# Optimization experiments

Measured on AMD Instinct MI355X. Metric: run time of the kernel, lower is better.

## Reference

```python
import jax, jax.numpy as jnp
import numpy as np

NUM_FREQS = 10
Z_SIZE = 256
HIDDEN = 256
N_LAYERS = 8
N_POLY = 100000
PE_DIM = 2 * NUM_FREQS + 2 * NUM_FREQS * 2 + 4  # 64
IN1 = PE_DIM + Z_SIZE        # 320
IN_MID = HIDDEN + IN1        # 576
SLOPE = 0.01


def setup_inputs() -> dict:
    key = jax.random.key(0)
    ks = jax.random.split(key, 12)
    B = 131072
    xy = jax.random.normal(ks[0], (B, 2), dtype=jnp.float32)
    idx = jax.random.randint(ks[1], (B,), 0, N_POLY, dtype=jnp.int64 if jax.config.jax_enable_x64 else jnp.int32)
    emb = jax.random.normal(ks[2], (N_POLY, Z_SIZE), dtype=jnp.float32) * 0.01
    s = 0.02
    W1a = jax.random.normal(ks[3], (IN1, HIDDEN), dtype=jnp.float32) * s
    b1a = jnp.zeros((HIDDEN,), jnp.float32)
    W1b = jax.random.normal(ks[4], (HIDDEN, HIDDEN), dtype=jnp.float32) * s
    b1b = jnp.zeros((HIDDEN,), jnp.float32)
    Wa = jax.random.normal(ks[5], (N_LAYERS, IN_MID, HIDDEN), dtype=jnp.float32) * s
    ba = jnp.zeros((N_LAYERS, HIDDEN), jnp.float32)
    Wb = jax.random.normal(ks[6], (N_LAYERS, HIDDEN, HIDDEN), dtype=jnp.float32) * s
    bb = jnp.zeros((N_LAYERS, HIDDEN), jnp.float32)
    W2 = jax.random.normal(ks[7], (HIDDEN, 1), dtype=jnp.float32) * s
    b2 = jnp.zeros((1,), jnp.float32)
    return {"xy": xy, "idx": idx, "emb": emb, "W1a": W1a, "b1a": b1a,
            "W1b": W1b, "b1b": b1b, "Wa": Wa, "ba": ba, "Wb": Wb, "bb": bb,
            "W2": W2, "b2": b2}


def _pos_encode(xy):
    # linspace freq bands (log_sampling=False default)
    freq = jnp.linspace(1.0, 6.0, NUM_FREQS).astype(xy.dtype)  # (F,)
    xf = xy[:, None, :] * freq[:, None]                         # (B,F,2)
    # cat([x_input, sin, cos], dim=1) then reshape -> (B, (1+2F)*2)
    out = jnp.concatenate([xy[:, None, :], jnp.sin(xf), jnp.cos(xf)], axis=1)
    out = out.reshape(xy.shape[0], -1)                          # (B,42)
    # polar fourier encoding
    r = jnp.sqrt(xy[:, 0] ** 2 + xy[:, 1] ** 2)                 # (B,)
    rf = r[:, None] * freq                                      # (B,F)
    pe = jnp.concatenate([xy, jnp.sin(rf), jnp.cos(rf)], axis=-1)  # (B,22)
    return jnp.concatenate([out, pe], axis=-1)                  # (B,64)


def reference(xy, idx, emb, W1a, b1a, W1b, b1b, Wa, ba, Wb, bb, W2, b2):
    feat = _pos_encode(xy)                       # (B,64)
    z = emb[idx]                                 # (B,256)
    xy_z = jnp.concatenate([feat, z], axis=1)    # (B,320)
    x = jax.nn.leaky_relu(xy_z @ W1a + b1a, SLOPE) @ W1b + b1b  # (B,256)
    for i in range(N_LAYERS):
        h = jnp.concatenate([xy_z, x], axis=1)   # (B,576)
        x = jax.nn.leaky_relu(h @ Wa[i] + ba[i], SLOPE) @ Wb[i] + bb[i]
    return x @ W2 + b2                           # (B,1)
```

## Files before the change

### kernel.cpp

```cpp
#include <hip/hip_runtime.h>
#include <hip/hip_bf16.h>


typedef __attribute__((ext_vector_type(8))) __bf16 bfv8;
typedef __attribute__((ext_vector_type(8))) short s16x8;
typedef __attribute__((ext_vector_type(4))) float f32x4;
typedef __attribute__((ext_vector_type(4))) int i32x4;

__device__ __forceinline__ short f2bf(float f) {
  unsigned u = __builtin_bit_cast(unsigned, f);
  u = (u + 0x7fffu + ((u >> 16) & 1u)) >> 16;
  return (short)u;
}
__device__ __forceinline__ float bf2f(short s) {
  unsigned u = ((unsigned)(unsigned short)s) << 16;
  return __builtin_bit_cast(float, u);
}
__device__ __forceinline__ int swzaddr(int base, int stride, int row, int colbyte) {
  return base + row * stride + (colbyte ^ (((row & 7) << 4) ^ ((row & 8) << 2)));
}
__device__ __forceinline__ void ldsbar() {
  __builtin_amdgcn_sched_barrier(0);
  asm volatile("s_waitcnt lgkmcnt(0)");
  __builtin_amdgcn_s_barrier();
  __builtin_amdgcn_sched_barrier(0);
}

__global__ void pack_weights_kernel(const float* __restrict__ W1a, const float* __restrict__ W1b,
                                    const float* __restrict__ Wa, const float* __restrict__ Wb,
                                    short* __restrict__ ws) {
  int p = blockIdx.x * blockDim.x + threadIdx.x;
  const int P1 = 10240;
  const int P2 = P1 + 8192;
  const int P3 = P2 + 8 * 18432;
  const int P4 = P3 + 8 * 8192;
  if (p >= P4) return;
  const float* src;
  int q;
  if (p < P1)      { src = W1a; q = p; }
  else if (p < P2) { src = W1b; q = p - P1; }
  else if (p < P3) { q = p - P2; int l = q / 18432; q -= l * 18432; src = Wa + l * 147456; }
  else             { q = p - P3; int l = q / 8192;  q -= l * 8192;  src = Wb + l * 65536; }
  const int lane = q & 63, t = q >> 6, nt = t & 15, kt = t >> 4;
  const int k0 = kt * 32 + ((lane >> 4) << 3);
  const int n  = ((nt >> 1) << 5) + ((lane & 15) << 1) + (nt & 1);
  short* dst = ws + (size_t)p * 8;
#pragma unroll
  for (int i = 0; i < 8; ++i) dst[i] = f2bf(src[(size_t)(k0 + i) * 256 + n]);
}

struct BPre { bfv8 b0, b1; };
struct AFrag { bfv8 r0, r1, r2, r3; };

__device__ __forceinline__ bfv8 bfrag(const short* __restrict__ wp, int kt, int nt, int lane) {
  const short* base = wp + (((size_t)(kt * 16 + nt)) << 9);
  return *(const bfv8*)(base + (lane << 3));
}

template<int NKT, int SPLITKT, bool LEAKY>
__device__ __forceinline__ BPre do_gemm(short* lds,
    int a1Base, int a1S, int a2Base, int a2S,
    const short* __restrict__ wp, const short* __restrict__ wpn,
    const float* __restrict__ bias, int outBase,
    int wc, int lane, BPre pre)
{
  const int lo = lane & 15, hi = lane >> 4;
  const int ntb = wc << 1;
  const float2 bv = *(const float2*)(bias + (wc << 5) + (lo << 1));
  f32x4 acc[4][2];
#pragma unroll
  for (int r = 0; r < 4; ++r) { acc[r][0] = (f32x4)0.f; acc[r][1] = (f32x4)0.f; }

  const int xr  = ((lo & 7) << 4) ^ ((lo & 8) << 2);
  const int hib = hi << 4;
  const char* A1E = (const char*)lds + a1Base + lo * a1S + ((     hib) ^ xr);
  const char* A1O = (const char*)lds + a1Base + lo * a1S + ((64 + hib) ^ xr);
  const char* A2E = (const char*)lds + a2Base + lo * a2S + ((     hib) ^ xr);
  const char* A2O = (const char*)lds + a2Base + lo * a2S + ((64 + hib) ^ xr);

  auto aLoad = [&](int kt, AFrag& dst) {
    const bool g1 = kt < SPLITKT;
    const int kk  = g1 ? kt : kt - SPLITKT;
    const int st  = g1 ? a1S : a2S;
    const char* b = (g1 ? ((kk & 1) ? A1O : A1E) : ((kk & 1) ? A2O : A2E)) + (kk >> 1) * 128;
    dst.r0 = *(const bfv8*)(b);
    dst.r1 = *(const bfv8*)(b + (st << 4));
    dst.r2 = *(const bfv8*)(b + (st << 5));
    dst.r3 = *(const bfv8*)(b + (st << 4) * 3);
  };

  bfv8 bst[4][2];
  AFrag ast[3];
  bst[0][0] = pre.b0; bst[0][1] = pre.b1;
  if (NKT > 1) { bst[1][0] = bfrag(wp, 1, ntb, lane); bst[1][1] = bfrag(wp, 1, ntb + 1, lane); }
  if (NKT > 2) { bst[2][0] = bfrag(wp, 2, ntb, lane); bst[2][1] = bfrag(wp, 2, ntb + 1, lane); }
  aLoad(0, ast[0]);
  if (NKT > 1) aLoad(1, ast[1]);
  BPre nxt;

#pragma unroll
  for (int i = 0; i < NKT; ++i) {
    if (i + 3 < NKT) {
      bst[(i + 3) & 3][0] = bfrag(wp, i + 3, ntb, lane);
      bst[(i + 3) & 3][1] = bfrag(wp, i + 3, ntb + 1, lane);
    } else if (i + 3 == NKT || (NKT <= 3 && i == 0)) {
      nxt.b0 = bfrag(wpn, 0, ntb, lane);
      nxt.b1 = bfrag(wpn, 0, ntb + 1, lane);
    }
    if (i + 2 < NKT) aLoad(i + 2, ast[(i + 2) % 3]);
    const AFrag& ac = ast[i % 3];
    __builtin_amdgcn_s_setprio(1);
    acc[0][0] = __builtin_amdgcn_mfma_f32_16x16x32_bf16(ac.r0, bst[i & 3][0], acc[0][0], 0, 0, 0);
    acc[0][1] = __builtin_amdgcn_mfma_f32_16x16x32_bf16(ac.r0, bst[i & 3][1], acc[0][1], 0, 0, 0);
    acc[1][0] = __builtin_amdgcn_mfma_f32_16x16x32_bf16(ac.r1, bst[i & 3][0], acc[1][0], 0, 0, 0);
    acc[1][1] = __builtin_amdgcn_mfma_f32_16x16x32_bf16(ac.r1, bst[i & 3][1], acc[1][1], 0, 0, 0);
    acc[2][0] = __builtin_amdgcn_mfma_f32_16x16x32_bf16(ac.r2, bst[i & 3][0], acc[2][0], 0, 0, 0);
    acc[2][1] = __builtin_amdgcn_mfma_f32_16x16x32_bf16(ac.r2, bst[i & 3][1], acc[2][1], 0, 0, 0);
    acc[3][0] = __builtin_amdgcn_mfma_f32_16x16x32_bf16(ac.r3, bst[i & 3][0], acc[3][0], 0, 0, 0);
    acc[3][1] = __builtin_amdgcn_mfma_f32_16x16x32_bf16(ac.r3, bst[i & 3][1], acc[3][1], 0, 0, 0);
    __builtin_amdgcn_s_setprio(0);
  }
#pragma unroll
  for (int rt = 0; rt < 4; ++rt)
#pragma unroll
    for (int rr = 0; rr < 4; ++rr) {
      float v0 = acc[rt][0][rr] + bv.x;
      float v1 = acc[rt][1][rr] + bv.y;
      if (LEAKY) { v0 = fmaxf(v0, 0.01f * v0); v1 = fmaxf(v1, 0.01f * v1); }
      unsigned pk;
      asm("v_cvt_pk_bf16_f32 %0, %1, %2" : "=v"(pk) : "v"(v0), "v"(v1));
      const int orow = (rt << 4) + (hi << 2) + rr;
      *(unsigned*)((char*)lds + swzaddr(outBase, 512, orow, (wc << 6) + (lo << 2))) = pk;
    }
  return nxt;
}

__launch_bounds__(512, 1)
__global__ void geo2vec_kernel(const float* __restrict__ xy, const int* __restrict__ idx,
    const float* __restrict__ emb,
    const float* __restrict__ b1a, const float* __restrict__ b1b,
    const float* __restrict__ ba, const float* __restrict__ bb,
    const float* __restrict__ W2, const float* __restrict__ b2,
    const short* __restrict__ wp, float* __restrict__ out)
{
  __shared__ short lds[53248];
  const int tid = threadIdx.x;
  const int lane = tid & 63;
  const int wc = __builtin_amdgcn_readfirstlane(tid >> 6);

  BPre pre;
  pre.b0 = bfrag(wp, 0, (wc << 1), lane);
  pre.b1 = bfrag(wp, 0, (wc << 1) + 1, lane);

  {
    const int g = tid >> 3, j = tid & 7;
    const int row = blockIdx.x * 64 + g;
    const float xv = xy[2 * row], yv = xy[2 * row + 1];
    const float rv = sqrtf(xv * xv + yv * yv);
    union { short s[8]; i32x4 v; } tmp;
#pragma unroll
    for (int i = 0; i < 8; ++i) {
      const int c = 8 * j + i;
      float fv;
      if (c < 2)       fv = c ? yv : xv;
      else if (c < 22) { int m = c - 2;  float f = 1.0f + (5.0f / 9.0f) * (m >> 1); fv = sinf(((m & 1) ? yv : xv) * f); }
      else if (c < 42) { int m = c - 22; float f = 1.0f + (5.0f / 9.0f) * (m >> 1); fv = cosf(((m & 1) ? yv : xv) * f); }
      else if (c < 44) fv = (c == 42) ? xv : yv;
      else if (c < 54) fv = sinf(rv * (1.0f + (5.0f / 9.0f) * (c - 44)));
      else             fv = cosf(rv * (1.0f + (5.0f / 9.0f) * (c - 54)));
      tmp.s[i] = f2bf(fv);
    }
    *(i32x4*)((char*)lds + swzaddr(0, 640, g, j << 4)) = tmp.v;
    const float* zr = emb + (size_t)(unsigned)idx[row] * 256;
#pragma unroll
    for (int c4 = 0; c4 < 4; ++c4) {
      const int cel = j * 32 + c4 * 8;
      const float4 f0 = *(const float4*)(zr + cel);
      const float4 f1 = *(const float4*)(zr + cel + 4);
      union { short s[8]; i32x4 v; } t2;
      t2.s[0] = f2bf(f0.x); t2.s[1] = f2bf(f0.y); t2.s[2] = f2bf(f0.z); t2.s[3] = f2bf(f0.w);
      t2.s[4] = f2bf(f1.x); t2.s[5] = f2bf(f1.y); t2.s[6] = f2bf(f1.z); t2.s[7] = f2bf(f1.w);
      *(i32x4*)((char*)lds + swzaddr(0, 640, g, (64 + cel) << 1)) = t2.v;
    }
  }
  ldsbar();

  pre = do_gemm<10, 10, true >(lds, 0, 640, 0, 640,         wp,         wp + 81920,  b1a, 73728, wc, lane, pre);
  ldsbar();
  pre = do_gemm<8,  8,  false>(lds, 73728, 512, 73728, 512, wp + 81920, wp + 147456, b1b, 40960, wc, lane, pre);
  ldsbar();
  for (int l = 0; l < 8; ++l) {
    const short* wa = wp + 147456 + l * 147456;
    const short* wb = wp + 1327104 + l * 65536;
    const short* wan = (l < 7) ? (wa + 147456) : wp;
    pre = do_gemm<18, 10, true >(lds, 0, 640, 40960, 512,     wa, wb,  ba + l * 256, 73728, wc, lane, pre);
    ldsbar();
    pre = do_gemm<8,  8,  false>(lds, 73728, 512, 73728, 512, wb, wan, bb + l * 256, 40960, wc, lane, pre);
    ldsbar();
  }
  {
    const int r = tid >> 3, j = tid & 7;
    float sum = 0.f;
#pragma unroll
    for (int h = 0; h < 4; ++h) {
      const int cb = 64 * j + 16 * h;
      const s16x8 v = *(const s16x8*)((const char*)lds + swzaddr(40960, 512, r, cb));
      const int c0 = 32 * j + 8 * h;
      const float4 w0 = *(const float4*)(W2 + c0);
      const float4 w1 = *(const float4*)(W2 + c0 + 4);
      sum += bf2f(v[0]) * w0.x + bf2f(v[1]) * w0.y + bf2f(v[2]) * w0.z + bf2f(v[3]) * w0.w;
      sum += bf2f(v[4]) * w1.x + bf2f(v[5]) * w1.y + bf2f(v[6]) * w1.z + bf2f(v[7]) * w1.w;
    }
    sum += __shfl_xor(sum, 1); sum += __shfl_xor(sum, 2); sum += __shfl_xor(sum, 4);
    if (j == 0) out[blockIdx.x * 64 + r] = sum + b2[0];
  }
}

extern "C" void kernel_launch(void* const* d_in, const int* in_sizes, int n_in,
                              void* d_out, int out_size, void* d_ws, size_t ws_size,
                              hipStream_t stream) {
  const float* xy  = (const float*)d_in[0];
  const int*   idx = (const int*)d_in[1];
  const float* emb = (const float*)d_in[2];
  const float* W1a = (const float*)d_in[3];
  const float* b1a = (const float*)d_in[4];
  const float* W1b = (const float*)d_in[5];
  const float* b1b = (const float*)d_in[6];
  const float* Wa  = (const float*)d_in[7];
  const float* ba  = (const float*)d_in[8];
  const float* Wb  = (const float*)d_in[9];
  const float* bb  = (const float*)d_in[10];
  const float* W2  = (const float*)d_in[11];
  const float* b2  = (const float*)d_in[12];
  short* ws = (short*)d_ws;
  const int B = in_sizes[1];

  hipLaunchKernelGGL(pack_weights_kernel, dim3(904), dim3(256), 0, stream,
                     W1a, W1b, Wa, Wb, ws);
  hipLaunchKernelGGL(geo2vec_kernel, dim3(B / 64), dim3(512), 0, stream,
                     xy, idx, emb, b1a, b1b, ba, bb, W2, b2, ws, (float*)d_out);
}
```

Baseline: 475.3 us.

## Move post-Wb barrier into mid-GEMM and preload first A fragment across stages

The barrier after each Wb GEMM is removed. A barrier is now placed inside the following Wa GEMM at the point where it switches from the static xy_z operand to the freshly written x operand. The Wb GEMM also preloads the first A fragment of the xy_z block from LDS and hands it to the next Wa GEMM. This lets waves start the Wa layer on static inputs without waiting for all waves to finish writing x, overlapping barrier skew with useful MFMA work. It relies on the xy_z region never being overwritten and on the barrier placement (SPLITKT-2, with prefetch depth two) covering every read of x.

```diff
diff --git a/kernel.cpp b/kernel.cpp
--- a/kernel.cpp
+++ b/kernel.cpp
@@ -51,18 +51,19 @@
 
 struct BPre { bfv8 b0, b1; };
 struct AFrag { bfv8 r0, r1, r2, r3; };
+struct Pre { BPre b; AFrag a; };
 
 __device__ __forceinline__ bfv8 bfrag(const short* __restrict__ wp, int kt, int nt, int lane) {
   const short* base = wp + (((size_t)(kt * 16 + nt)) << 9);
   return *(const bfv8*)(base + (lane << 3));
 }
 
-template<int NKT, int SPLITKT, bool LEAKY>
-__device__ __forceinline__ BPre do_gemm(short* lds,
+template<int NKT, int SPLITKT, bool LEAKY, bool MIDBAR, bool PRE_A, bool PRE_NEXT_A>
+__device__ __forceinline__ Pre do_gemm(short* lds,
     int a1Base, int a1S, int a2Base, int a2S,
     const short* __restrict__ wp, const short* __restrict__ wpn,
     const float* __restrict__ bias, int outBase,
-    int wc, int lane, BPre pre)
+    int wc, int lane, Pre pre)
 {
   const int lo = lane & 15, hi = lane >> 4;
   const int ntb = wc << 1;
@@ -91,23 +92,31 @@
 
   bfv8 bst[4][2];
   AFrag ast[3];
-  bst[0][0] = pre.b0; bst[0][1] = pre.b1;
+  bst[0][0] = pre.b.b0; bst[0][1] = pre.b.b1;
   if (NKT > 1) { bst[1][0] = bfrag(wp, 1, ntb, lane); bst[1][1] = bfrag(wp, 1, ntb + 1, lane); }
   if (NKT > 2) { bst[2][0] = bfrag(wp, 2, ntb, lane); bst[2][1] = bfrag(wp, 2, ntb + 1, lane); }
-  aLoad(0, ast[0]);
+  if (PRE_A) ast[0] = pre.a; else aLoad(0, ast[0]);
   if (NKT > 1) aLoad(1, ast[1]);
-  BPre nxt;
+  Pre nxt;
 
 #pragma unroll
   for (int i = 0; i < NKT; ++i) {
+    if (MIDBAR && i == SPLITKT - 2) ldsbar();
     if (i + 3 < NKT) {
       bst[(i + 3) & 3][0] = bfrag(wp, i + 3, ntb, lane);
       bst[(i + 3) & 3][1] = bfrag(wp, i + 3, ntb + 1, lane);
     } else if (i + 3 == NKT || (NKT <= 3 && i == 0)) {
-      nxt.b0 = bfrag(wpn, 0, ntb, lane);
-      nxt.b1 = bfrag(wpn, 0, ntb + 1, lane);
+      nxt.b.b0 = bfrag(wpn, 0, ntb, lane);
+      nxt.b.b1 = bfrag(wpn, 0, ntb + 1, lane);
     }
     if (i + 2 < NKT) aLoad(i + 2, ast[(i + 2) % 3]);
+    if (PRE_NEXT_A && i == NKT - 1) {
+      const char* bx = (const char*)lds + lo * 640 + (hib ^ xr);
+      nxt.a.r0 = *(const bfv8*)(bx);
+      nxt.a.r1 = *(const bfv8*)(bx + 640 * 16);
+      nxt.a.r2 = *(const bfv8*)(bx + 640 * 32);
+      nxt.a.r3 = *(const bfv8*)(bx + 640 * 48);
+    }
     const AFrag& ac = ast[i % 3];
     __builtin_amdgcn_s_setprio(1);
     acc[0][0] = __builtin_amdgcn_mfma_f32_16x16x32_bf16(ac.r0, bst[i & 3][0], acc[0][0], 0, 0, 0);
@@ -148,9 +157,9 @@
   const int lane = tid & 63;
   const int wc = __builtin_amdgcn_readfirstlane(tid >> 6);
 
-  BPre pre;
-  pre.b0 = bfrag(wp, 0, (wc << 1), lane);
-  pre.b1 = bfrag(wp, 0, (wc << 1) + 1, lane);
+  Pre pre;
+  pre.b.b0 = bfrag(wp, 0, (wc << 1), lane);
+  pre.b.b1 = bfrag(wp, 0, (wc << 1) + 1, lane);
 
   {
     const int g = tid >> 3, j = tid & 7;
@@ -185,19 +194,23 @@
   }
   ldsbar();
 
-  pre = do_gemm<10, 10, true >(lds, 0, 640, 0, 640,         wp,         wp + 81920,  b1a, 73728, wc, lane, pre);
+  pre = do_gemm<10, 10, true,  false, false, false>(lds, 0, 640, 0, 640,
+        wp, wp + 81920, b1a, 73728, wc, lane, pre);
   ldsbar();
-  pre = do_gemm<8,  8,  false>(lds, 73728, 512, 73728, 512, wp + 81920, wp + 147456, b1b, 40960, wc, lane, pre);
-  ldsbar();
+  pre = do_gemm<8, 8, false, false, false, true>(lds, 73728, 512, 73728, 512,
+        wp + 81920, wp + 147456, b1b, 40960, wc, lane, pre);
   for (int l = 0; l < 8; ++l) {
     const short* wa = wp + 147456 + l * 147456;
     const short* wb = wp + 1327104 + l * 65536;
     const short* wan = (l < 7) ? (wa + 147456) : wp;
-    pre = do_gemm<18, 10, true >(lds, 0, 640, 40960, 512,     wa, wb,  ba + l * 256, 73728, wc, lane, pre);
+    pre = do_gemm<18, 10, true, true, true, false>(lds, 0, 640, 40960, 512,
+          wa, wb, ba + l * 256, 73728, wc, lane, pre);
     ldsbar();
-    pre = do_gemm<8,  8,  false>(lds, 73728, 512, 73728, 512, wb, wan, bb + l * 256, 40960, wc, lane, pre);
-    ldsbar();
-  }
+    pre = do_gemm<8, 8, false, false, false, true>(lds, 73728, 512, 73728, 512,
+          wb, wan, bb + l * 256, 40960, wc, lane, pre);
+  }
+  ldsbar();
+
   {
     const int r = tid >> 3, j = tid & 7;
     float sum = 0.f;
```

Result: no change. 472.5 us (-0.6%).

## Split-K the wide layer GEMMs across wave pairs with LDS partial-sum exchange

Applied to the files above, without the earlier changes.

The 8 waves of the wide (concat-input) GEMMs are reorganised as 2 K-halves by 4 column groups. Each wave now computes 64 output columns over half the reduction dimension, which halves the per-wave LDS reads of the A operand while keeping the weight-fragment loads unchanged. The two halves swap partial sums through a new LDS staging area before bias, leaky-ReLU and the bf16 store. This costs more LDS, an extra barrier and a bf16-rounded partial sum, which adds some numerical error. The narrow GEMMs keep their layout but now prefetch the next wide layer's split-K weight fragments.

```diff
diff --git a/kernel.cpp b/kernel.cpp
--- a/kernel.cpp
+++ b/kernel.cpp
@@ -49,7 +49,11 @@
   for (int i = 0; i < 8; ++i) dst[i] = f2bf(src[(size_t)(k0 + i) * 256 + n]);
 }
 
-struct BPre { bfv8 b0, b1; };
+#define XB 40960
+#define TB 73728
+#define SG 106496
+
+struct Pre { bfv8 q0, q1, q2, q3; };
 struct AFrag { bfv8 r0, r1, r2, r3; };
 
 __device__ __forceinline__ bfv8 bfrag(const short* __restrict__ wp, int kt, int nt, int lane) {
@@ -57,31 +61,24 @@
   return *(const bfv8*)(base + (lane << 3));
 }
 
-template<int NKT, int SPLITKT, bool LEAKY>
-__device__ __forceinline__ BPre do_gemm(short* lds,
-    int a1Base, int a1S, int a2Base, int a2S,
+template<int KT0, int KT1, int SPLITKT>
+__device__ __forceinline__ void khalf_a(const short* lds,
     const short* __restrict__ wp, const short* __restrict__ wpn,
-    const float* __restrict__ bias, int outBase,
-    int wc, int lane, BPre pre)
+    int ntb, int nxntb, int lane, f32x4 (&acc)[4][4], Pre pre, Pre& nxt)
 {
+  constexpr int H = KT1 - KT0;
   const int lo = lane & 15, hi = lane >> 4;
-  const int ntb = wc << 1;
-  const float2 bv = *(const float2*)(bias + (wc << 5) + (lo << 1));
-  f32x4 acc[4][2];
-#pragma unroll
-  for (int r = 0; r < 4; ++r) { acc[r][0] = (f32x4)0.f; acc[r][1] = (f32x4)0.f; }
-
   const int xr  = ((lo & 7) << 4) ^ ((lo & 8) << 2);
   const int hib = hi << 4;
-  const char* A1E = (const char*)lds + a1Base + lo * a1S + ((     hib) ^ xr);
-  const char* A1O = (const char*)lds + a1Base + lo * a1S + ((64 + hib) ^ xr);
-  const char* A2E = (const char*)lds + a2Base + lo * a2S + ((     hib) ^ xr);
-  const char* A2O = (const char*)lds + a2Base + lo * a2S + ((64 + hib) ^ xr);
+  const char* A1E = (const char*)lds + lo * 640 + ((     hib) ^ xr);
+  const char* A1O = (const char*)lds + lo * 640 + ((64 + hib) ^ xr);
+  const char* A2E = (const char*)lds + XB + lo * 512 + ((     hib) ^ xr);
+  const char* A2O = (const char*)lds + XB + lo * 512 + ((64 + hib) ^ xr);
 
   auto aLoad = [&](int kt, AFrag& dst) {
     const bool g1 = kt < SPLITKT;
     const int kk  = g1 ? kt : kt - SPLITKT;
-    const int st  = g1 ? a1S : a2S;
+    const int st  = g1 ? 640 : 512;
     const char* b = (g1 ? ((kk & 1) ? A1O : A1E) : ((kk & 1) ? A2O : A2E)) + (kk >> 1) * 128;
     dst.r0 = *(const bfv8*)(b);
     dst.r1 = *(const bfv8*)(b + (st << 4));
@@ -89,26 +86,142 @@
     dst.r3 = *(const bfv8*)(b + (st << 4) * 3);
   };
 
+  bfv8 bst[3][4];
+  AFrag ast[2];
+  bst[0][0] = pre.q0; bst[0][1] = pre.q1; bst[0][2] = pre.q2; bst[0][3] = pre.q3;
+  if (H > 1) {
+#pragma unroll
+    for (int c = 0; c < 4; ++c) bst[1][c] = bfrag(wp, KT0 + 1, ntb + c, lane);
+  }
+  aLoad(KT0, ast[0]);
+
+#pragma unroll
+  for (int i = 0; i < H; ++i) {
+    const int kt = KT0 + i;
+    if (i + 2 < H) {
+#pragma unroll
+      for (int c = 0; c < 4; ++c) bst[(i + 2) % 3][c] = bfrag(wp, kt + 2, ntb + c, lane);
+    } else if (i + 2 == H) {
+      nxt.q0 = bfrag(wpn, 0, nxntb, lane);
+      nxt.q1 = bfrag(wpn, 0, nxntb + 1, lane);
+    }
+    if (i + 1 < H) aLoad(kt + 1, ast[(i + 1) & 1]);
+    const AFrag& ac = ast[i & 1];
+    __builtin_amdgcn_s_setprio(1);
+#pragma unroll
+    for (int ct = 0; ct < 4; ++ct) {
+      acc[0][ct] = __builtin_amdgcn_mfma_f32_16x16x32_bf16(ac.r0, bst[i % 3][ct], acc[0][ct], 0, 0, 0);
+      acc[1][ct] = __builtin_amdgcn_mfma_f32_16x16x32_bf16(ac.r1, bst[i % 3][ct], acc[1][ct], 0, 0, 0);
+      acc[2][ct] = __builtin_amdgcn_mfma_f32_16x16x32_bf16(ac.r2, bst[i % 3][ct], acc[2][ct], 0, 0, 0);
+      acc[3][ct] = __builtin_amdgcn_mfma_f32_16x16x32_bf16(ac.r3, bst[i % 3][ct], acc[3][ct], 0, 0, 0);
+    }
+    __builtin_amdgcn_s_setprio(0);
+  }
+}
+
+template<int NKT, int SPLITKT, int H0>
+__device__ __forceinline__ Pre do_gemm_a(short* lds,
+    const short* __restrict__ wp, const short* __restrict__ wpn,
+    const float* __restrict__ bias, int ks, int cg, int w, int lane, Pre pre)
+{
+  const int lo = lane & 15, hi = lane >> 4;
+  const int ntb = cg << 2, nxntb = w << 1;
+  const float2 bv = *(const float2*)(bias + (cg << 6) + (ks << 5) + (lo << 1));
+  f32x4 acc[4][4];
+#pragma unroll
+  for (int r = 0; r < 4; ++r)
+#pragma unroll
+    for (int c = 0; c < 4; ++c) acc[r][c] = (f32x4)0.f;
+
+  Pre nxt;
+  if (ks == 0) khalf_a<0, H0, SPLITKT>(lds, wp, wpn, ntb, nxntb, lane, acc, pre, nxt);
+  else         khalf_a<H0, NKT, SPLITKT>(lds, wp, wpn, ntb, nxntb, lane, acc, pre, nxt);
+
+  char* stg = (char*)lds + SG;
+  const int wslot = ((ks << 8) + (cg << 6) + lane) << 4;
+  const int rslot = (((ks ^ 1) << 8) + (cg << 6) + lane) << 4;
+  const int dp = (ks ^ 1) << 1;
+  const int op = ks << 1;
+#pragma unroll
+  for (int rt = 0; rt < 4; ++rt) {
+    i32x4 d;
+#pragma unroll
+    for (int rr = 0; rr < 4; ++rr) {
+      unsigned pk;
+      asm("v_cvt_pk_bf16_f32 %0, %1, %2" : "=v"(pk) : "v"(acc[rt][dp][rr]), "v"(acc[rt][dp + 1][rr]));
+      d[rr] = (int)pk;
+    }
+    *(i32x4*)(stg + rt * 8192 + wslot) = d;
+  }
+  ldsbar();
+#pragma unroll
+  for (int rt = 0; rt < 4; ++rt) {
+    const i32x4 pk = *(const i32x4*)(stg + rt * 8192 + rslot);
+#pragma unroll
+    for (int rr = 0; rr < 4; ++rr) {
+      const unsigned u = (unsigned)pk[rr];
+      const float p0 = __builtin_bit_cast(float, u << 16);
+      const float p1 = __builtin_bit_cast(float, u & 0xffff0000u);
+      float v0 = acc[rt][op][rr]     + p0 + bv.x;
+      float v1 = acc[rt][op + 1][rr] + p1 + bv.y;
+      v0 = fmaxf(v0, 0.01f * v0); v1 = fmaxf(v1, 0.01f * v1);
+      unsigned o;
+      asm("v_cvt_pk_bf16_f32 %0, %1, %2" : "=v"(o) : "v"(v0), "v"(v1));
+      const int orow = (rt << 4) + (hi << 2) + rr;
+      *(unsigned*)((char*)lds + swzaddr(TB, 512, orow, (cg << 7) + (ks << 6) + (lo << 2))) = o;
+    }
+  }
+  ldsbar();
+  return nxt;
+}
+
+__device__ __forceinline__ Pre do_gemm_b(short* lds,
+    const short* __restrict__ wp, const short* __restrict__ wpn, int nxkt0,
+    const float* __restrict__ bias, int w, int ks, int cg, int lane, Pre pre)
+{
+  constexpr int NKT = 8;
+  const int lo = lane & 15, hi = lane >> 4;
+  const int ntb = w << 1;
+  const float2 bv = *(const float2*)(bias + (w << 5) + (lo << 1));
+  f32x4 acc[4][2];
+#pragma unroll
+  for (int r = 0; r < 4; ++r) { acc[r][0] = (f32x4)0.f; acc[r][1] = (f32x4)0.f; }
+
+  const int xr  = ((lo & 7) << 4) ^ ((lo & 8) << 2);
+  const int hib = hi << 4;
+  const char* AE = (const char*)lds + TB + lo * 512 + ((     hib) ^ xr);
+  const char* AO = (const char*)lds + TB + lo * 512 + ((64 + hib) ^ xr);
+
+  auto aLoad = [&](int kt, AFrag& dst) {
+    const char* b = ((kt & 1) ? AO : AE) + (kt >> 1) * 128;
+    dst.r0 = *(const bfv8*)(b);
+    dst.r1 = *(const bfv8*)(b + (512 << 4));
+    dst.r2 = *(const bfv8*)(b + (512 << 5));
+    dst.r3 = *(const bfv8*)(b + (512 << 4) * 3);
+  };
+
   bfv8 bst[4][2];
-  AFrag ast[3];
-  bst[0][0] = pre.b0; bst[0][1] = pre.b1;
-  if (NKT > 1) { bst[1][0] = bfrag(wp, 1, ntb, lane); bst[1][1] = bfrag(wp, 1, ntb + 1, lane); }
-  if (NKT > 2) { bst[2][0] = bfrag(wp, 2, ntb, lane); bst[2][1] = bfrag(wp, 2, ntb + 1, lane); }
+  AFrag ast[2];
+  bst[0][0] = pre.q0; bst[0][1] = pre.q1;
+  bst[1][0] = bfrag(wp, 1, ntb, lane); bst[1][1] = bfrag(wp, 1, ntb + 1, lane);
+  bst[2][0] = bfrag(wp, 2, ntb, lane); bst[2][1] = bfrag(wp, 2, ntb + 1, lane);
   aLoad(0, ast[0]);
-  if (NKT > 1) aLoad(1, ast[1]);
-  BPre nxt;
+  Pre nxt;
 
 #pragma unroll
   for (int i = 0; i < NKT; ++i) {
     if (i + 3 < NKT) {
       bst[(i + 3) & 3][0] = bfrag(wp, i + 3, ntb, lane);
       bst[(i + 3) & 3][1] = bfrag(wp, i + 3, ntb + 1, lane);
-    } else if (i + 3 == NKT || (NKT <= 3 && i == 0)) {
-      nxt.b0 = bfrag(wpn, 0, ntb, lane);
-      nxt.b1 = bfrag(wpn, 0, ntb + 1, lane);
-    }
-    if (i + 2 < NKT) aLoad(i + 2, ast[(i + 2) % 3]);
-    const AFrag& ac = ast[i % 3];
+    } else if (i + 3 == NKT) {
+      const int na = cg << 2;
+      nxt.q0 = bfrag(wpn, nxkt0, na, lane);
+      nxt.q1 = bfrag(wpn, nxkt0, na + 1, lane);
+      nxt.q2 = bfrag(wpn, nxkt0, na + 2, lane);
+      nxt.q3 = bfrag(wpn, nxkt0, na + 3, lane);
+    }
+    if (i + 1 < NKT) aLoad(i + 1, ast[(i + 1) & 1]);
+    const AFrag& ac = ast[i & 1];
     __builtin_amdgcn_s_setprio(1);
     acc[0][0] = __builtin_amdgcn_mfma_f32_16x16x32_bf16(ac.r0, bst[i & 3][0], acc[0][0], 0, 0, 0);
     acc[0][1] = __builtin_amdgcn_mfma_f32_16x16x32_bf16(ac.r0, bst[i & 3][1], acc[0][1], 0, 0, 0);
@@ -124,13 +237,12 @@
   for (int rt = 0; rt < 4; ++rt)
 #pragma unroll
     for (int rr = 0; rr < 4; ++rr) {
-      float v0 = acc[rt][0][rr] + bv.x;
-      float v1 = acc[rt][1][rr] + bv.y;
-      if (LEAKY) { v0 = fmaxf(v0, 0.01f * v0); v1 = fmaxf(v1, 0.01f * v1); }
+      const float v0 = acc[rt][0][rr] + bv.x;
+      const float v1 = acc[rt][1][rr] + bv.y;
       unsigned pk;
       asm("v_cvt_pk_bf16_f32 %0, %1, %2" : "=v"(pk) : "v"(v0), "v"(v1));
       const int orow = (rt << 4) + (hi << 2) + rr;
-      *(unsigned*)((char*)lds + swzaddr(outBase, 512, orow, (wc << 6) + (lo << 2))) = pk;
+      *(unsigned*)((char*)lds + swzaddr(XB, 512, orow, (w << 6) + (lo << 2))) = pk;
     }
   return nxt;
 }
@@ -143,14 +255,17 @@
     const float* __restrict__ W2, const float* __restrict__ b2,
     const short* __restrict__ wp, float* __restrict__ out)
 {
-  __shared__ short lds[53248];
+  __shared__ short lds[69632];
   const int tid = threadIdx.x;
   const int lane = tid & 63;
-  const int wc = __builtin_amdgcn_readfirstlane(tid >> 6);
-
-  BPre pre;
-  pre.b0 = bfrag(wp, 0, (wc << 1), lane);
-  pre.b1 = bfrag(wp, 0, (wc << 1) + 1, lane);
+  const int w  = __builtin_amdgcn_readfirstlane(tid >> 6);
+  const int ks = w >> 2, cg = w & 3;
+
+  Pre pre;
+  pre.q0 = bfrag(wp, ks * 5, (cg << 2), lane);
+  pre.q1 = bfrag(wp, ks * 5, (cg << 2) + 1, lane);
+  pre.q2 = bfrag(wp, ks * 5, (cg << 2) + 2, lane);
+  pre.q3 = bfrag(wp, ks * 5, (cg << 2) + 3, lane);
 
   {
     const int g = tid >> 3, j = tid & 7;
@@ -185,17 +300,15 @@
   }
   ldsbar();
 
-  pre = do_gemm<10, 10, true >(lds, 0, 640, 0, 640,         wp,         wp + 81920,  b1a, 73728, wc, lane, pre);
-  ldsbar();
-  pre = do_gemm<8,  8,  false>(lds, 73728, 512, 73728, 512, wp + 81920, wp + 147456, b1b, 40960, wc, lane, pre);
+  pre = do_gemm_a<10, 10, 5>(lds, wp, wp + 81920, b1a, ks, cg, w, lane, pre);
+  pre = do_gemm_b(lds, wp + 81920, wp + 147456, ks * 9, b1b, w, ks, cg, lane, pre);
   ldsbar();
   for (int l = 0; l < 8; ++l) {
     const short* wa = wp + 147456 + l * 147456;
     const short* wb = wp + 1327104 + l * 65536;
     const short* wan = (l < 7) ? (wa + 147456) : wp;
-    pre = do_gemm<18, 10, true >(lds, 0, 640, 40960, 512,     wa, wb,  ba + l * 256, 73728, wc, lane, pre);
-    ldsbar();
-    pre = do_gemm<8,  8,  false>(lds, 73728, 512, 73728, 512, wb, wan, bb + l * 256, 40960, wc, lane, pre);
+    pre = do_gemm_a<18, 10, 9>(lds, wa, wb, ba + l * 256, ks, cg, w, lane, pre);
+    pre = do_gemm_b(lds, wb, wan, ks * 9, bb + l * 256, w, ks, cg, lane, pre);
     ldsbar();
   }
   {
@@ -204,7 +317,7 @@
 #pragma unroll
     for (int h = 0; h < 4; ++h) {
       const int cb = 64 * j + 16 * h;
-      const s16x8 v = *(const s16x8*)((const char*)lds + swzaddr(40960, 512, r, cb));
+      const s16x8 v = *(const s16x8*)((const char*)lds + swzaddr(XB, 512, r, cb));
       const int c0 = 32 * j + 8 * h;
       const float4 w0 = *(const float4*)(W2 + c0);
       const float4 w1 = *(const float4*)(W2 + c0 + 4);
```

Result: slower. 995.5 us (+109.5%).
